# Kernel tuning notes

Hardware: AMD Instinct MI355X
Metric: run time of the kernel (lower is better)

## Reference

```python
import jax, jax.numpy as jnp
import numpy as np

N, E, H, L = 50000, 1_600_000, 128, 3


def _ln(x, g, b, eps=1e-5):
    m = x.mean(-1, keepdims=True)
    v = x.var(-1, keepdims=True)
    return (x - m) / jnp.sqrt(v + eps) * g + b


def _mlp2(inp, w1, b1, g, be, w2, b2):
    # Linear -> LayerNorm -> SiLU -> (Dropout=identity in eval) -> Linear
    h = inp @ w1 + b1
    h = jax.nn.silu(_ln(h, g, be))
    return h @ w2 + b2


def setup_inputs() -> dict:
    key = jax.random.key(0)
    ks = jax.random.split(key, 16)
    s = 0.05
    inp = {
        'x': jax.random.normal(ks[0], (N, 7), jnp.float32),
        'pos': jax.random.normal(ks[1], (N, 3), jnp.float32),
        'edge_index': jax.random.randint(ks[2], (2, E), 0, N, jnp.int64),
        'enc_w1': jax.random.normal(ks[3], (7, H)) * s,
        'enc_b1': jnp.zeros((H,)),
        'enc_g': jnp.ones((H,)),
        'enc_be': jnp.zeros((H,)),
        'enc_w2': jax.random.normal(ks[4], (H, H)) * s,
        'enc_b2': jnp.zeros((H,)),
        'e_w1': jax.random.normal(ks[5], (L, 2 * H + 5, H)) * s,
        'e_b1': jnp.zeros((L, H)),
        'e_g': jnp.ones((L, H)),
        'e_be': jnp.zeros((L, H)),
        'e_w2': jax.random.normal(ks[6], (L, H, H)) * s,
        'e_b2': jnp.zeros((L, H)),
        'n_w1': jax.random.normal(ks[7], (L, 2 * H, H)) * s,
        'n_b1': jnp.zeros((L, H)),
        'n_g': jnp.ones((L, H)),
        'n_be': jnp.zeros((L, H)),
        'n_w2': jax.random.normal(ks[8], (L, H, H)) * s,
        'n_b2': jnp.zeros((L, H)),
        'ln_g': jnp.ones((L, H)),
        'ln_b': jnp.zeros((L, H)),
        'dec_w1': jax.random.normal(ks[9], (H, H)) * s,
        'dec_b1': jnp.zeros((H,)),
        'dec_w2': jax.random.normal(ks[10], (H, H // 2)) * s,
        'dec_b2': jnp.zeros((H // 2,)),
        'dec_w3': jax.random.normal(ks[11], (H // 2, 6)) * s,
        'dec_b3': jnp.zeros((6,)),
    }
    return inp


def reference(x, pos, edge_index, enc_w1, enc_b1, enc_g, enc_be, enc_w2, enc_b2,
              e_w1, e_b1, e_g, e_be, e_w2, e_b2,
              n_w1, n_b1, n_g, n_be, n_w2, n_b2,
              ln_g, ln_b, dec_w1, dec_b1, dec_w2, dec_b2, dec_w3, dec_b3):
    n_nodes = x.shape[0]
    row, col = edge_index[0], edge_index[1]  # row=source(j), col=target(i)

    # physics edge features: [dist, direction(3), 1/r^2]
    diff = pos[col] - pos[row]                          # (E,3)
    dist = jnp.linalg.norm(diff, axis=-1, keepdims=True) + 1e-8
    edge_attr = jnp.concatenate([dist, diff / dist, 1.0 / (dist ** 2 + 1e-6)], -1)

    h = _mlp2(x, enc_w1, enc_b1, enc_g, enc_be, enc_w2, enc_b2)  # (N,H)

    for l in range(L):
        # message: cat(x_i, x_j, edge_attr) -> edge MLP
        msg_in = jnp.concatenate([h[col], h[row], edge_attr], -1)  # (E,2H+5)
        msg = _mlp2(msg_in, e_w1[l], e_b1[l], e_g[l], e_be[l], e_w2[l], e_b2[l])
        # scatter-add aggregate to targets
        aggr = jax.ops.segment_sum(msg, col, num_segments=n_nodes)  # (N,H)
        # update: cat(x, aggr) -> node MLP, then residual + LayerNorm
        h_new = _mlp2(jnp.concatenate([h, aggr], -1),
                      n_w1[l], n_b1[l], n_g[l], n_be[l], n_w2[l], n_b2[l])
        h = _ln(h + h_new, ln_g[l], ln_b[l])

    d = jax.nn.silu(h @ dec_w1 + dec_b1)
    d = jax.nn.silu(d @ dec_w2 + dec_b2)
    delta = d @ dec_w3 + dec_b3                                  # (N,6)
    return x[:, :6] + delta
```

## Files before the change

### kernel.cpp

```cpp
#include <hip/hip_runtime.h>

typedef unsigned short u16;
typedef unsigned int u32;
typedef __bf16 bf16x8 __attribute__((ext_vector_type(8)));
typedef float f32x4 __attribute__((ext_vector_type(4)));
typedef float f32x2 __attribute__((ext_vector_type(2)));

#define AS_STRIDE 136

__device__ __forceinline__ u16 f2bf1(float f) {
  union { __bf16 h; u16 u; } c; c.h = (__bf16)f; return c.u;
}
__device__ __forceinline__ u32 cvt2bf(float a, float b) {
  union { __bf16 h[2]; u32 u; } c; c.h[0] = (__bf16)a; c.h[1] = (__bf16)b; return c.u;
}
__device__ __forceinline__ float bf2f(u16 u) {
  union { u32 u; float f; } v; v.u = ((u32)u) << 16; return v.f;
}
__device__ __forceinline__ float silu_f(float a) {
  return a * __builtin_amdgcn_rcpf(1.f + __expf(-a));
}
__device__ __forceinline__ float rsq_f(float x) {
  return __builtin_amdgcn_rsqf(x);
}
__device__ __forceinline__ f32x2 unpk2(u32 p) {
  union { u32 u; float f; } a, b;
  a.u = p << 16; b.u = p & 0xffff0000u;
  return (f32x2){a.f, b.f};
}
__device__ __forceinline__ int permP(int i) {
  return ((i >> 2) & 3) * 16 + ((i >> 4) & 3) * 4 + (i & 3);
}

__global__ void edge_hist(const int* __restrict__ edst, int E, int* __restrict__ cnt) {
  int i = blockIdx.x * blockDim.x + threadIdx.x;
  if (i < E) atomicAdd(&cnt[edst[i]], 1);
}

__global__ __launch_bounds__(1024)
void scan_kernel(const int* __restrict__ cnt, int* __restrict__ cursor, int Nn) {
  __shared__ int part[1024];
  int t = threadIdx.x;
  int per = (Nn + 1023) / 1024;
  int b = t * per;
  int s = 0;
  for (int i = 0; i < per; i++) { int idx = b + i; if (idx < Nn) s += cnt[idx]; }
  part[t] = s;
  __syncthreads();
  for (int d = 1; d < 1024; d <<= 1) {
    int v = (t >= d) ? part[t - d] : 0;
    __syncthreads();
    part[t] += v;
    __syncthreads();
  }
  int excl = (t == 0) ? 0 : part[t - 1];
  for (int i = 0; i < per; i++) {
    int idx = b + i;
    if (idx < Nn) { cursor[idx] = excl; excl += cnt[idx]; }
  }
}

__global__ void edge_scatter(const int* __restrict__ esrc, const int* __restrict__ edst,
                             int E, int* __restrict__ cursor,
                             int* __restrict__ ssrc, int* __restrict__ sdst) {
  int i = blockIdx.x * blockDim.x + threadIdx.x;
  if (i < E) {
    int d = edst[i];
    int p = atomicAdd(&cursor[d], 1);
    ssrc[p] = esrc[i];
    sdst[p] = d;
  }
}

__global__ void prep_weights(const float* __restrict__ e_w1, const float* __restrict__ e_w2,
                             const float* __restrict__ n_w1, const float* __restrict__ n_w2,
                             u16* __restrict__ eW1T, u16* __restrict__ eW2T,
                             u16* __restrict__ nW1T, u16* __restrict__ nW2T) {
  int i = blockIdx.x * blockDim.x + threadIdx.x;
  const int s1 = 3 * 128 * 256;
  const int s2 = 3 * 128 * 128;
  if (i < s1) {
    int l = i / 32768, r = i % 32768, n = r >> 8, k = r & 255;
    eW1T[i] = f2bf1(e_w1[l * 33408 + k * 128 + n]);
  } else if (i < s1 + s2) {
    int j = i - s1; int l = j / 16384, r = j % 16384, n = r >> 7, k = r & 127;
    eW2T[j] = f2bf1(e_w2[l * 16384 + k * 128 + n]);
  } else if (i < s1 + s2 + s1) {
    int j = i - s1 - s2; int l = j / 32768, r = j % 32768, n = r >> 8, k = r & 255;
    nW1T[j] = f2bf1(n_w1[l * 32768 + k * 128 + n]);
  } else if (i < 2 * s1 + 2 * s2) {
    int j = i - 2 * s1 - s2; int l = j / 16384, r = j % 16384, n = r >> 7, k = r & 127;
    nW2T[j] = f2bf1(n_w2[l * 16384 + k * 128 + n]);
  }
}

__global__ void prep_weights2(const float* __restrict__ enc_w1, const float* __restrict__ enc_w2,
                              const float* __restrict__ dec_w1, const float* __restrict__ dec_w2,
                              const float* __restrict__ dec_w3,
                              u16* __restrict__ encW1T, u16* __restrict__ encW2T,
                              u16* __restrict__ decW1T, u16* __restrict__ decW2T,
                              u16* __restrict__ decW3T) {
  int i = blockIdx.x * blockDim.x + threadIdx.x;
  if (i < 4096) {
    int n = i >> 5, k = i & 31;
    encW1T[i] = (k < 7) ? f2bf1(enc_w1[k * 128 + n]) : (u16)0;
  } else if (i < 20480) {
    int j = i - 4096; int n = j >> 7, k = j & 127;
    encW2T[j] = f2bf1(enc_w2[k * 128 + n]);
  } else if (i < 36864) {
    int j = i - 20480; int n = j >> 7, k = j & 127;
    decW1T[j] = f2bf1(dec_w1[k * 128 + n]);
  } else if (i < 45056) {
    int j = i - 36864; int n = j >> 7, k = j & 127;
    decW2T[j] = f2bf1(dec_w2[k * 64 + n]);
  } else if (i < 46080) {
    int j = i - 45056; int n = j >> 6, k = j & 63;
    decW3T[j] = (n < 6) ? f2bf1(dec_w3[k * 6 + n]) : (u16)0;
  }
}

__global__ __launch_bounds__(256, 4)
void encoder_mfma(const float* __restrict__ x,
                  const u16* __restrict__ W1T,
                  const float* __restrict__ b1,
                  const float* __restrict__ g, const float* __restrict__ be,
                  const u16* __restrict__ W2T,
                  const float* __restrict__ b2,
                  const u16* __restrict__ eW1T0,
                  const float* __restrict__ eb10,
                  u16* __restrict__ hbf, u16* __restrict__ hd_all,
                  u16* __restrict__ hs_all, int Nn) {
  __shared__ __align__(16) u16 As[64 * 40];
  __shared__ __align__(16) u16 ts[64 * AS_STRIDE];
  const int tid = threadIdx.x;
  const int m0 = blockIdx.x * 64;
  const int w = tid >> 6, lane = tid & 63, quad = lane >> 4, l16 = lane & 15;
  const int c0w = w * 32;

  if (tid < 64) {
    int node = m0 + tid; if (node >= Nn) node = Nn - 1;
    union { u16 us[32]; uint4 v[4]; } pk;
    #pragma unroll
    for (int k = 0; k < 32; k++) pk.us[k] = 0;
    #pragma unroll
    for (int k = 0; k < 7; k++) pk.us[k] = f2bf1(x[node * 7 + k]);
    #pragma unroll
    for (int k = 0; k < 4; k++) *(uint4*)(As + tid * 40 + k * 8) = pk.v[k];
  }
  __syncthreads();

  f32x4 acc[4][2];
  #pragma unroll
  for (int rt = 0; rt < 4; rt++)
    #pragma unroll
    for (int ct = 0; ct < 2; ct++)
      acc[rt][ct] = (f32x4){0.f, 0.f, 0.f, 0.f};
  {
    const int kl = quad * 8;
    bf16x8 af[4];
    #pragma unroll
    for (int rt = 0; rt < 4; rt++)
      af[rt] = *(const bf16x8*)(As + (rt * 16 + l16) * 40 + kl);
    #pragma unroll
    for (int ct = 0; ct < 2; ct++) {
      bf16x8 bfv = *(const bf16x8*)(W1T + (c0w + ct * 16 + l16) * 32 + kl);
      #pragma unroll
      for (int rt = 0; rt < 4; rt++)
        acc[rt][ct] = __builtin_amdgcn_mfma_f32_16x16x32_bf16(af[rt], bfv, acc[rt][ct], 0, 0, 0);
    }
  }
  #pragma unroll
  for (int ct = 0; ct < 2; ct++) {
    int n = c0w + ct * 16 + l16;
    float b1v = b1[n];
    #pragma unroll
    for (int rt = 0; rt < 4; rt++)
      #pragma unroll
      for (int r = 0; r < 4; r++)
        ts[(rt * 16 + quad * 4 + r) * AS_STRIDE + n] = f2bf1(acc[rt][ct][r] + b1v);
  }
  __syncthreads();

  {
    int row = tid >> 2, sub = tid & 3;
    float s = 0.f, sq = 0.f, vals[32];
    #pragma unroll
    for (int i = 0; i < 32; i++) {
      float v = bf2f(ts[row * AS_STRIDE + sub + i * 4]);
      vals[i] = v; s += v; sq += v * v;
    }
    s += __shfl_xor(s, 1); sq += __shfl_xor(sq, 1);
    s += __shfl_xor(s, 2); sq += __shfl_xor(sq, 2);
    float mean = s * (1.f / 128.f);
    float rstd = rsq_f(sq * (1.f / 128.f) - mean * mean + 1e-5f);
    #pragma unroll
    for (int i = 0; i < 32; i++) {
      int c = sub + i * 4;
      float a = (vals[i] - mean) * rstd * g[c] + be[c];
      ts[row * AS_STRIDE + c] = f2bf1(silu_f(a));
    }
  }
  __syncthreads();

  f32x4 acc2[4][2];
  #pragma unroll
  for (int rt = 0; rt < 4; rt++)
    #pragma unroll
    for (int ct = 0; ct < 2; ct++)
      acc2[rt][ct] = (f32x4){0.f, 0.f, 0.f, 0.f};
  #pragma unroll
  for (int kk = 0; kk < 4; kk++) {
    const int kl = kk * 32 + quad * 8;
    bf16x8 af[4];
    #pragma unroll
    for (int rt = 0; rt < 4; rt++)
      af[rt] = *(const bf16x8*)(ts + (rt * 16 + l16) * AS_STRIDE + kl);
    #pragma unroll
    for (int ct = 0; ct < 2; ct++) {
      bf16x8 bfv = *(const bf16x8*)(W2T + (size_t)(c0w + ct * 16 + l16) * 128 + kl);
      #pragma unroll
      for (int rt = 0; rt < 4; rt++)
        acc2[rt][ct] = __builtin_amdgcn_mfma_f32_16x16x32_bf16(af[rt], bfv, acc2[rt][ct], 0, 0, 0);
    }
  }
  __syncthreads();
  #pragma unroll
  for (int ct = 0; ct < 2; ct++) {
    int n = c0w + ct * 16 + l16;
    float b2v = b2[n];
    #pragma unroll
    for (int rt = 0; rt < 4; rt++)
      #pragma unroll
      for (int r = 0; r < 4; r++) {
        int m = rt * 16 + quad * 4 + r;
        int node = m0 + m;
        u16 hb = f2bf1(acc2[rt][ct][r] + b2v);
        ts[m * AS_STRIDE + n] = hb;
        if (node < Nn) hbf[(size_t)node * 128 + n] = hb;
      }
  }
  __syncthreads();

  {
    f32x4 ah[4][2];
    #pragma unroll
    for (int rt = 0; rt < 4; rt++)
      #pragma unroll
      for (int ct = 0; ct < 2; ct++)
        ah[rt][ct] = (f32x4){0.f, 0.f, 0.f, 0.f};
    #pragma unroll
    for (int kk = 0; kk < 4; kk++) {
      const int kl = kk * 32 + quad * 8;
      bf16x8 af[4];
      #pragma unroll
      for (int rt = 0; rt < 4; rt++)
        af[rt] = *(const bf16x8*)(ts + (rt * 16 + l16) * AS_STRIDE + kl);
      #pragma unroll
      for (int ct = 0; ct < 2; ct++) {
        bf16x8 bd = *(const bf16x8*)(eW1T0 + (size_t)(c0w + ct * 16 + l16) * 256 + kl);
        #pragma unroll
        for (int rt = 0; rt < 4; rt++)
          ah[rt][ct] = __builtin_amdgcn_mfma_f32_16x16x32_bf16(af[rt], bd, ah[rt][ct], 0, 0, 0);
      }
    }
    #pragma unroll
    for (int ct = 0; ct < 2; ct++) {
      int n = c0w + ct * 16 + l16;
      float b1v = eb10[n];
      #pragma unroll
      for (int rt = 0; rt < 4; rt++)
        #pragma unroll
        for (int r = 0; r < 4; r++) {
          int node = m0 + rt * 16 + quad * 4 + r;
          if (node < Nn) hd_all[(size_t)node * 128 + n] = f2bf1(ah[rt][ct][r] + b1v);
        }
    }
    #pragma unroll
    for (int rt = 0; rt < 4; rt++)
      #pragma unroll
      for (int ct = 0; ct < 2; ct++)
        ah[rt][ct] = (f32x4){0.f, 0.f, 0.f, 0.f};
    #pragma unroll
    for (int kk = 0; kk < 4; kk++) {
      const int kl = kk * 32 + quad * 8;
      bf16x8 af[4];
      #pragma unroll
      for (int rt = 0; rt < 4; rt++)
        af[rt] = *(const bf16x8*)(ts + (rt * 16 + l16) * AS_STRIDE + kl);
      #pragma unroll
      for (int ct = 0; ct < 2; ct++) {
        bf16x8 bs = *(const bf16x8*)(eW1T0 + (size_t)(c0w + ct * 16 + l16) * 256 + 128 + kl);
        #pragma unroll
        for (int rt = 0; rt < 4; rt++)
          ah[rt][ct] = __builtin_amdgcn_mfma_f32_16x16x32_bf16(af[rt], bs, ah[rt][ct], 0, 0, 0);
      }
    }
    #pragma unroll
    for (int ct = 0; ct < 2; ct++) {
      int n = c0w + ct * 16 + l16;
      #pragma unroll
      for (int rt = 0; rt < 4; rt++)
        #pragma unroll
        for (int r = 0; r < 4; r++) {
          int node = m0 + rt * 16 + quad * 4 + r;
          if (node < Nn) hs_all[(size_t)node * 128 + n] = f2bf1(ah[rt][ct][r]);
        }
    }
  }
}

__global__ __launch_bounds__(256, 6)
void edge_mlp_kernel(const int* __restrict__ ssrc, const int* __restrict__ sdst,
                     const float* __restrict__ pos,
                     const u16* __restrict__ hd_all, const u16* __restrict__ hs_all,
                     const float* __restrict__ w1cF,
                     const float* __restrict__ g, const float* __restrict__ be,
                     const u16* __restrict__ W2T,
                     const float* __restrict__ b2,
                     float* __restrict__ aggr) {
  __shared__ int s_dst[64];
  __shared__ __align__(16) float s_ea[64 * 8];
  __shared__ __align__(16) float s_w1c[5 * 128];
  __shared__ __align__(16) u16 s_t[64 * AS_STRIDE];

  const int tid = threadIdx.x;
  const int bid = blockIdx.x;
  const int e0 = ((bid & 7) * (gridDim.x >> 3) + (bid >> 3)) * 64;
  const int w = tid >> 6, lane = tid & 63, quad = lane >> 4, l16 = lane & 15;
  const int c0w = w * 32;
  const int rg = tid >> 4, cg = tid & 15;
  const int c0 = cg * 8;

  int pdst[4], psrc[4];
  #pragma unroll
  for (int rr = 0; rr < 4; rr++) {
    int j = permP(rg * 4 + rr);
    pdst[rr] = sdst[e0 + j];
    psrc[rr] = ssrc[e0 + j];
  }
  uint4 hd4[4], hs4[4];
  #pragma unroll
  for (int rr = 0; rr < 4; rr++) {
    hd4[rr] = *(const uint4*)(hd_all + (size_t)pdst[rr] * 128 + c0);
    hs4[rr] = *(const uint4*)(hs_all + (size_t)psrc[rr] * 128 + c0);
  }
  asm volatile("" ::: "memory");

  if (tid < 64) {
    int jp = permP(tid);
    int src = ssrc[e0 + jp], dst = sdst[e0 + jp];
    s_dst[tid] = sdst[e0 + tid];
    float dx = pos[dst * 3 + 0] - pos[src * 3 + 0];
    float dy = pos[dst * 3 + 1] - pos[src * 3 + 1];
    float dz = pos[dst * 3 + 2] - pos[src * 3 + 2];
    float dist = sqrtf(dx * dx + dy * dy + dz * dz) + 1e-8f;
    float inv = __builtin_amdgcn_rcpf(dist);
    s_ea[tid * 8 + 0] = dist;
    s_ea[tid * 8 + 1] = dx * inv;
    s_ea[tid * 8 + 2] = dy * inv;
    s_ea[tid * 8 + 3] = dz * inv;
    s_ea[tid * 8 + 4] = __builtin_amdgcn_rcpf(dist * dist + 1e-6f);
  }
  if (tid < 160) *(float4*)(s_w1c + tid * 4) = *(const float4*)(w1cF + tid * 4);
  __syncthreads();

  {
    f32x2 t2a[4][4];
    #pragma unroll
    for (int rr = 0; rr < 4; rr++) {
      u32 hp[4] = {hd4[rr].x, hd4[rr].y, hd4[rr].z, hd4[rr].w};
      u32 sp[4] = {hs4[rr].x, hs4[rr].y, hs4[rr].z, hs4[rr].w};
      #pragma unroll
      for (int p = 0; p < 4; p++)
        t2a[rr][p] = unpk2(hp[p]) + unpk2(sp[p]);
    }
    #pragma unroll
    for (int k = 0; k < 5; k++) {
      f32x4 wa = *(const f32x4*)(s_w1c + k * 128 + c0);
      f32x4 wb = *(const f32x4*)(s_w1c + k * 128 + c0 + 4);
      f32x2 wk0 = (f32x2){wa[0], wa[1]}, wk1 = (f32x2){wa[2], wa[3]};
      f32x2 wk2 = (f32x2){wb[0], wb[1]}, wk3 = (f32x2){wb[2], wb[3]};
      #pragma unroll
      for (int rr = 0; rr < 4; rr++) {
        float e = s_ea[(rg * 4 + rr) * 8 + k];
        f32x2 ev = (f32x2){e, e};
        t2a[rr][0] += ev * wk0;
        t2a[rr][1] += ev * wk1;
        t2a[rr][2] += ev * wk2;
        t2a[rr][3] += ev * wk3;
      }
    }
    f32x2 g2[4], be2[4];
    {
      f32x4 ga = *(const f32x4*)(g + c0), gb = *(const f32x4*)(g + c0 + 4);
      f32x4 ba = *(const f32x4*)(be + c0), bb = *(const f32x4*)(be + c0 + 4);
      g2[0] = (f32x2){ga[0], ga[1]}; g2[1] = (f32x2){ga[2], ga[3]};
      g2[2] = (f32x2){gb[0], gb[1]}; g2[3] = (f32x2){gb[2], gb[3]};
      be2[0] = (f32x2){ba[0], ba[1]}; be2[1] = (f32x2){ba[2], ba[3]};
      be2[2] = (f32x2){bb[0], bb[1]}; be2[3] = (f32x2){bb[2], bb[3]};
    }
    #pragma unroll
    for (int rr = 0; rr < 4; rr++) {
      int m = rg * 4 + rr;
      f32x2 sm2 = (f32x2){0.f, 0.f}, sq2 = (f32x2){0.f, 0.f};
      #pragma unroll
      for (int p = 0; p < 4; p++) {
        sm2 += t2a[rr][p];
        sq2 += t2a[rr][p] * t2a[rr][p];
      }
      float sm = sm2[0] + sm2[1], sq = sq2[0] + sq2[1];
      sm += __shfl_xor(sm, 1);  sq += __shfl_xor(sq, 1);
      sm += __shfl_xor(sm, 2);  sq += __shfl_xor(sq, 2);
      sm += __shfl_xor(sm, 4);  sq += __shfl_xor(sq, 4);
      sm += __shfl_xor(sm, 8);  sq += __shfl_xor(sq, 8);
      float mean = sm * (1.f / 128.f);
      float rstd = rsq_f(sq * (1.f / 128.f) - mean * mean + 1e-5f);
      f32x2 sc = (f32x2){rstd, rstd};
      f32x2 ofs = (f32x2){-mean * rstd, -mean * rstd};
      float o[8];
      #pragma unroll
      for (int p = 0; p < 4; p++) {
        f32x2 a = t2a[rr][p] * sc + ofs;
        a = a * g2[p] + be2[p];
        o[2 * p]     = silu_f(a[0]);
        o[2 * p + 1] = silu_f(a[1]);
      }
      uint4 st;
      st.x = cvt2bf(o[0], o[1]); st.y = cvt2bf(o[2], o[3]);
      st.z = cvt2bf(o[4], o[5]); st.w = cvt2bf(o[6], o[7]);
      *(uint4*)(s_t + m * AS_STRIDE + c0) = st;
    }
  }
  __syncthreads();

  f32x4 acc2[4][2];
  #pragma unroll
  for (int rt = 0; rt < 4; rt++)
    #pragma unroll
    for (int ct = 0; ct < 2; ct++)
      acc2[rt][ct] = (f32x4){0.f, 0.f, 0.f, 0.f};

  #pragma unroll
  for (int kk = 0; kk < 4; kk++) {
    const int kl = kk * 32 + quad * 8;
    bf16x8 af[4];
    #pragma unroll
    for (int rt = 0; rt < 4; rt++)
      af[rt] = *(const bf16x8*)(s_t + (rt * 16 + l16) * AS_STRIDE + kl);
    #pragma unroll
    for (int ct = 0; ct < 2; ct++) {
      bf16x8 bfv = *(const bf16x8*)(W2T + (size_t)(c0w + ct * 16 + l16) * 128 + kl);
      #pragma unroll
      for (int rt = 0; rt < 4; rt++)
        acc2[rt][ct] = __builtin_amdgcn_mfma_f32_16x16x32_bf16(af[rt], bfv, acc2[rt][ct], 0, 0, 0);
    }
  }

  {
    int dv[16];
    #pragma unroll
    for (int j = 0; j < 16; j++) dv[j] = s_dst[quad * 16 + j];

    #pragma unroll
    for (int ct = 0; ct < 2; ct++) {
      const int n = c0w + ct * 16 + l16;
      const float b2v = b2[n];
      float* ap = aggr + n;
      int cur = dv[0];
      float run = 0.f;
      #pragma unroll
      for (int j = 0; j < 16; j++) {
        if (dv[j] != cur) {
          atomicAdd(ap + (size_t)cur * 128, run);
          run = 0.f; cur = dv[j];
        }
        run += acc2[j >> 2][ct][j & 3] + b2v;
      }
      atomicAdd(ap + (size_t)cur * 128, run);
    }
  }
}

__global__ __launch_bounds__(256, 4)
void node_mlp_kernel(u16* __restrict__ hbf, float* __restrict__ aggr,
                     const u16* __restrict__ W1T, const float* __restrict__ b1,
                     const float* __restrict__ g, const float* __restrict__ be,
                     const u16* __restrict__ W2T, const float* __restrict__ b2,
                     const float* __restrict__ lng, const float* __restrict__ lnb,
                     const u16* __restrict__ W1Tn, const float* __restrict__ b1n,
                     u16* __restrict__ hd_all, u16* __restrict__ hs_all,
                     const float* __restrict__ x,
                     const u16* __restrict__ dW1T, const float* __restrict__ db1,
                     const u16* __restrict__ dW2T, const float* __restrict__ db2,
                     const u16* __restrict__ dW3T, const float* __restrict__ db3,
                     float* __restrict__ out,
                     int Nn) {
  __shared__ __align__(16) u16 As[128 * AS_STRIDE];
  u16* t_su = As;
  u16* u_su = As + 64 * AS_STRIDE;

  const int tid = threadIdx.x;
  const int m0 = blockIdx.x * 64;
  const int w = tid >> 6, lane = tid & 63, quad = lane >> 4, l16 = lane & 15;
  const int c0w = w * 32;

  {
    int r = tid >> 4, c8 = (tid & 15) * 8;
    const float4 z4 = {0.f, 0.f, 0.f, 0.f};
    #pragma unroll
    for (int rp = 0; rp < 4; rp++) {
      int m = rp * 16 + r;
      int node = m0 + m; if (node >= Nn) node = Nn - 1;
      *(uint4*)(As + m * AS_STRIDE + c8) = *(const uint4*)(hbf + (size_t)node * 128 + c8);
      float* ap = aggr + (size_t)node * 128 + c8;
      float4 f0 = *(const float4*)ap;
      float4 f1 = *(const float4*)(ap + 4);
      uint4 pk;
      pk.x = cvt2bf(f0.x, f0.y); pk.y = cvt2bf(f0.z, f0.w);
      pk.z = cvt2bf(f1.x, f1.y); pk.w = cvt2bf(f1.z, f1.w);
      *(uint4*)(As + (64 + m) * AS_STRIDE + c8) = pk;
      *(float4*)ap = z4;
      *(float4*)(ap + 4) = z4;
    }
  }
  __syncthreads();

  f32x4 acc[4][2];
  #pragma unroll
  for (int rt = 0; rt < 4; rt++)
    #pragma unroll
    for (int ct = 0; ct < 2; ct++)
      acc[rt][ct] = (f32x4){0.f, 0.f, 0.f, 0.f};

  #pragma unroll
  for (int kk = 0; kk < 8; kk++) {
    const u16* Ab = As + (kk < 4 ? 0 : 64 * AS_STRIDE);
    const int kl = (kk & 3) * 32 + quad * 8;
    bf16x8 af[4];
    #pragma unroll
    for (int rt = 0; rt < 4; rt++)
      af[rt] = *(const bf16x8*)(Ab + (rt * 16 + l16) * AS_STRIDE + kl);
    const int kg = kk * 32 + quad * 8;
    #pragma unroll
    for (int ct = 0; ct < 2; ct++) {
      bf16x8 bfv = *(const bf16x8*)(W1T + (size_t)(c0w + ct * 16 + l16) * 256 + kg);
      #pragma unroll
      for (int rt = 0; rt < 4; rt++)
        acc[rt][ct] = __builtin_amdgcn_mfma_f32_16x16x32_bf16(af[rt], bfv, acc[rt][ct], 0, 0, 0);
    }
  }

  float b1v[2];
  #pragma unroll
  for (int ct = 0; ct < 2; ct++) b1v[ct] = b1[c0w + ct * 16 + l16];
  __syncthreads();

  #pragma unroll
  for (int rt = 0; rt < 4; rt++)
    #pragma unroll
    for (int ct = 0; ct < 2; ct++) {
      int n = c0w + ct * 16 + l16;
      #pragma unroll
      for (int r = 0; r < 4; r++)
        t_su[(rt * 16 + quad * 4 + r) * AS_STRIDE + n] = f2bf1(acc[rt][ct][r] + b1v[ct]);
    }
  __syncthreads();

  {
    int row = tid >> 2, sub = tid & 3;
    float s = 0.f, sq = 0.f, vals[32];
    #pragma unroll
    for (int i = 0; i < 32; i++) {
      float v = bf2f(t_su[row * AS_STRIDE + sub + i * 4]);
      vals[i] = v; s += v; sq += v * v;
    }
    s += __shfl_xor(s, 1); sq += __shfl_xor(sq, 1);
    s += __shfl_xor(s, 2); sq += __shfl_xor(sq, 2);
    float mean = s * (1.f / 128.f);
    float rstd = rsq_f(sq * (1.f / 128.f) - mean * mean + 1e-5f);
    #pragma unroll
    for (int i = 0; i < 32; i++) {
      int c = sub + i * 4;
      float a = (vals[i] - mean) * rstd * g[c] + be[c];
      u_su[row * AS_STRIDE + c] = f2bf1(silu_f(a));
    }
  }
  __syncthreads();

  f32x4 acc2[4][2];
  #pragma unroll
  for (int rt = 0; rt < 4; rt++)
    #pragma unroll
    for (int ct = 0; ct < 2; ct++)
      acc2[rt][ct] = (f32x4){0.f, 0.f, 0.f, 0.f};

  #pragma unroll
  for (int kk = 0; kk < 4; kk++) {
    const int kl = kk * 32 + quad * 8;
    bf16x8 af[4];
    #pragma unroll
    for (int rt = 0; rt < 4; rt++)
      af[rt] = *(const bf16x8*)(u_su + (rt * 16 + l16) * AS_STRIDE + kl);
    #pragma unroll
    for (int ct = 0; ct < 2; ct++) {
      bf16x8 bfv = *(const bf16x8*)(W2T + (size_t)(c0w + ct * 16 + l16) * 128 + kl);
      #pragma unroll
      for (int rt = 0; rt < 4; rt++)
        acc2[rt][ct] = __builtin_amdgcn_mfma_f32_16x16x32_bf16(af[rt], bfv, acc2[rt][ct], 0, 0, 0);
    }
  }
  __syncthreads();

  #pragma unroll
  for (int ct = 0; ct < 2; ct++) {
    int n = c0w + ct * 16 + l16;
    float b2v = b2[n];
    #pragma unroll
    for (int rt = 0; rt < 4; rt++)
      #pragma unroll
      for (int r = 0; r < 4; r++) {
        int m = rt * 16 + quad * 4 + r;
        int node = m0 + m; if (node >= Nn) node = Nn - 1;
        t_su[m * AS_STRIDE + n] =
            f2bf1(acc2[rt][ct][r] + b2v + bf2f(hbf[(size_t)node * 128 + n]));
      }
  }
  __syncthreads();

  {
    int row = tid >> 2, sub = tid & 3;
    int node = m0 + row;
    float s = 0.f, sq = 0.f, vals[32];
    #pragma unroll
    for (int i = 0; i < 32; i++) {
      float v = bf2f(t_su[row * AS_STRIDE + sub + i * 4]);
      vals[i] = v; s += v; sq += v * v;
    }
    s += __shfl_xor(s, 1); sq += __shfl_xor(sq, 1);
    s += __shfl_xor(s, 2); sq += __shfl_xor(sq, 2);
    float mean = s * (1.f / 128.f);
    float rstd = rsq_f(sq * (1.f / 128.f) - mean * mean + 1e-5f);
    #pragma unroll
    for (int i = 0; i < 32; i++) {
      int c = sub + i * 4;
      float v = (vals[i] - mean) * rstd * lng[c] + lnb[c];
      u16 hb = f2bf1(v);
      t_su[row * AS_STRIDE + c] = hb;
      if (node < Nn) hbf[(size_t)node * 128 + c] = hb;
    }
  }

  if (W1Tn != nullptr) {
    __syncthreads();
    f32x4 ah[4][2];
    #pragma unroll
    for (int rt = 0; rt < 4; rt++)
      #pragma unroll
      for (int ct = 0; ct < 2; ct++)
        ah[rt][ct] = (f32x4){0.f, 0.f, 0.f, 0.f};
    #pragma unroll
    for (int kk = 0; kk < 4; kk++) {
      const int kl = kk * 32 + quad * 8;
      bf16x8 af[4];
      #pragma unroll
      for (int rt = 0; rt < 4; rt++)
        af[rt] = *(const bf16x8*)(t_su + (rt * 16 + l16) * AS_STRIDE + kl);
      #pragma unroll
      for (int ct = 0; ct < 2; ct++) {
        bf16x8 bd = *(const bf16x8*)(W1Tn + (size_t)(c0w + ct * 16 + l16) * 256 + kl);
        #pragma unroll
        for (int rt = 0; rt < 4; rt++)
          ah[rt][ct] = __builtin_amdgcn_mfma_f32_16x16x32_bf16(af[rt], bd, ah[rt][ct], 0, 0, 0);
      }
    }
    #pragma unroll
    for (int ct = 0; ct < 2; ct++) {
      int n = c0w + ct * 16 + l16;
      float bv = b1n[n];
      #pragma unroll
      for (int rt = 0; rt < 4; rt++)
        #pragma unroll
        for (int r = 0; r < 4; r++) {
          int node = m0 + rt * 16 + quad * 4 + r;
          if (node < Nn) hd_all[(size_t)node * 128 + n] = f2bf1(ah[rt][ct][r] + bv);
        }
    }
    #pragma unroll
    for (int rt = 0; rt < 4; rt++)
      #pragma unroll
      for (int ct = 0; ct < 2; ct++)
        ah[rt][ct] = (f32x4){0.f, 0.f, 0.f, 0.f};
    #pragma unroll
    for (int kk = 0; kk < 4; kk++) {
      const int kl = kk * 32 + quad * 8;
      bf16x8 af[4];
      #pragma unroll
      for (int rt = 0; rt < 4; rt++)
        af[rt] = *(const bf16x8*)(t_su + (rt * 16 + l16) * AS_STRIDE + kl);
      #pragma unroll
      for (int ct = 0; ct < 2; ct++) {
        bf16x8 bs = *(const bf16x8*)(W1Tn + (size_t)(c0w + ct * 16 + l16) * 256 + 128 + kl);
        #pragma unroll
        for (int rt = 0; rt < 4; rt++)
          ah[rt][ct] = __builtin_amdgcn_mfma_f32_16x16x32_bf16(af[rt], bs, ah[rt][ct], 0, 0, 0);
      }
    }
    #pragma unroll
    for (int ct = 0; ct < 2; ct++) {
      int n = c0w + ct * 16 + l16;
      #pragma unroll
      for (int rt = 0; rt < 4; rt++)
        #pragma unroll
        for (int r = 0; r < 4; r++) {
          int node = m0 + rt * 16 + quad * 4 + r;
          if (node < Nn) hs_all[(size_t)node * 128 + n] = f2bf1(ah[rt][ct][r]);
        }
    }
  }

  if (dW1T != nullptr) {
    __syncthreads();
    f32x4 da[4][2];
    #pragma unroll
    for (int rt = 0; rt < 4; rt++)
      #pragma unroll
      for (int ct = 0; ct < 2; ct++)
        da[rt][ct] = (f32x4){0.f, 0.f, 0.f, 0.f};
    #pragma unroll
    for (int kk = 0; kk < 4; kk++) {
      const int kl = kk * 32 + quad * 8;
      bf16x8 af[4];
      #pragma unroll
      for (int rt = 0; rt < 4; rt++)
        af[rt] = *(const bf16x8*)(t_su + (rt * 16 + l16) * AS_STRIDE + kl);
      #pragma unroll
      for (int ct = 0; ct < 2; ct++) {
        bf16x8 bfv = *(const bf16x8*)(dW1T + (size_t)(c0w + ct * 16 + l16) * 128 + kl);
        #pragma unroll
        for (int rt = 0; rt < 4; rt++)
          da[rt][ct] = __builtin_amdgcn_mfma_f32_16x16x32_bf16(af[rt], bfv, da[rt][ct], 0, 0, 0);
      }
    }
    __syncthreads();
    #pragma unroll
    for (int ct = 0; ct < 2; ct++) {
      int n = c0w + ct * 16 + l16;
      float bv = db1[n];
      #pragma unroll
      for (int rt = 0; rt < 4; rt++)
        #pragma unroll
        for (int r = 0; r < 4; r++)
          u_su[(rt * 16 + quad * 4 + r) * AS_STRIDE + n] = f2bf1(silu_f(da[rt][ct][r] + bv));
    }
    __syncthreads();
    {
      const int c0b = w * 16;
      f32x4 a2[4];
      #pragma unroll
      for (int rt = 0; rt < 4; rt++) a2[rt] = (f32x4){0.f, 0.f, 0.f, 0.f};
      #pragma unroll
      for (int kk = 0; kk < 4; kk++) {
        const int kl = kk * 32 + quad * 8;
        bf16x8 af[4];
        #pragma unroll
        for (int rt = 0; rt < 4; rt++)
          af[rt] = *(const bf16x8*)(u_su + (rt * 16 + l16) * AS_STRIDE + kl);
        bf16x8 bfv = *(const bf16x8*)(dW2T + (size_t)(c0b + l16) * 128 + kl);
        #pragma unroll
        for (int rt = 0; rt < 4; rt++)
          a2[rt] = __builtin_amdgcn_mfma_f32_16x16x32_bf16(af[rt], bfv, a2[rt], 0, 0, 0);
      }
      float bv = db2[c0b + l16];
      #pragma unroll
      for (int rt = 0; rt < 4; rt++)
        #pragma unroll
        for (int r = 0; r < 4; r++)
          t_su[(rt * 16 + quad * 4 + r) * 72 + c0b + l16] = f2bf1(silu_f(a2[rt][r] + bv));
    }
    __syncthreads();
    if (w == 0) {
      f32x4 a3[4];
      #pragma unroll
      for (int rt = 0; rt < 4; rt++) a3[rt] = (f32x4){0.f, 0.f, 0.f, 0.f};
      #pragma unroll
      for (int kk = 0; kk < 2; kk++) {
        const int kl = kk * 32 + quad * 8;
        bf16x8 af[4];
        #pragma unroll
        for (int rt = 0; rt < 4; rt++)
          af[rt] = *(const bf16x8*)(t_su + (rt * 16 + l16) * 72 + kl);
        bf16x8 bfv = *(const bf16x8*)(dW3T + l16 * 64 + kl);
        #pragma unroll
        for (int rt = 0; rt < 4; rt++)
          a3[rt] = __builtin_amdgcn_mfma_f32_16x16x32_bf16(af[rt], bfv, a3[rt], 0, 0, 0);
      }
      if (l16 < 6) {
        float bv = db3[l16];
        #pragma unroll
        for (int rt = 0; rt < 4; rt++)
          #pragma unroll
          for (int r = 0; r < 4; r++) {
            int node = m0 + rt * 16 + quad * 4 + r;
            if (node < Nn)
              out[(size_t)node * 6 + l16] = a3[rt][r] + bv + x[node * 7 + l16];
          }
      }
    }
  }
}

extern "C" void kernel_launch(void* const* d_in, const int* in_sizes, int n_in,
                              void* d_out, int out_size, void* d_ws, size_t ws_size,
                              hipStream_t stream) {
  const float* x      = (const float*)d_in[0];
  const float* pos    = (const float*)d_in[1];
  const int*   eidx   = (const int*)d_in[2];
  const float* enc_w1 = (const float*)d_in[3];
  const float* enc_b1 = (const float*)d_in[4];
  const float* enc_g  = (const float*)d_in[5];
  const float* enc_be = (const float*)d_in[6];
  const float* enc_w2 = (const float*)d_in[7];
  const float* enc_b2 = (const float*)d_in[8];
  const float* e_w1   = (const float*)d_in[9];
  const float* e_b1   = (const float*)d_in[10];
  const float* e_g    = (const float*)d_in[11];
  const float* e_be   = (const float*)d_in[12];
  const float* e_w2   = (const float*)d_in[13];
  const float* e_b2   = (const float*)d_in[14];
  const float* n_w1   = (const float*)d_in[15];
  const float* n_b1   = (const float*)d_in[16];
  const float* n_g    = (const float*)d_in[17];
  const float* n_be   = (const float*)d_in[18];
  const float* n_w2   = (const float*)d_in[19];
  const float* n_b2   = (const float*)d_in[20];
  const float* ln_g   = (const float*)d_in[21];
  const float* ln_b   = (const float*)d_in[22];
  const float* dec_w1 = (const float*)d_in[23];
  const float* dec_b1 = (const float*)d_in[24];
  const float* dec_w2 = (const float*)d_in[25];
  const float* dec_b2 = (const float*)d_in[26];
  const float* dec_w3 = (const float*)d_in[27];
  const float* dec_b3 = (const float*)d_in[28];

  const int N = in_sizes[0] / 7;
  const int E = in_sizes[2] / 2;

  char* ws = (char*)d_ws;
  size_t off = 0;
  u16*   hbf    = (u16*)(ws + off);   off += (size_t)N * 128 * 2;
  u16*   hd_all = (u16*)(ws + off);   off += (size_t)N * 128 * 2;
  u16*   hs_all = (u16*)(ws + off);   off += (size_t)N * 128 * 2;
  float* aggr   = (float*)(ws + off); off += (size_t)N * 128 * 4;
  u16* eW1T = (u16*)(ws + off); off += 3 * 128 * 256 * 2;
  u16* eW2T = (u16*)(ws + off); off += 3 * 128 * 128 * 2;
  u16* nW1T = (u16*)(ws + off); off += 3 * 128 * 256 * 2;
  u16* nW2T = (u16*)(ws + off); off += 3 * 128 * 128 * 2;
  u16* encW1T = (u16*)(ws + off); off += 128 * 32 * 2;
  u16* encW2T = (u16*)(ws + off); off += 128 * 128 * 2;
  u16* decW1T = (u16*)(ws + off); off += 128 * 128 * 2;
  u16* decW2T = (u16*)(ws + off); off += 64 * 128 * 2;
  u16* decW3T = (u16*)(ws + off); off += 16 * 64 * 2;
  int* cnt    = (int*)(ws + off); off += (size_t)N * 4;
  int* cursor = (int*)(ws + off); off += (size_t)N * 4;
  int* ssrc   = (int*)(ws + off); off += (size_t)E * 4;
  int* sdst   = (int*)(ws + off); off += (size_t)E * 4;

  hipMemsetAsync(cnt, 0, (size_t)N * 4, stream);
  edge_hist<<<(E + 255) / 256, 256, 0, stream>>>(eidx + E, E, cnt);
  scan_kernel<<<1, 1024, 0, stream>>>(cnt, cursor, N);
  edge_scatter<<<(E + 255) / 256, 256, 0, stream>>>(eidx, eidx + E, E, cursor, ssrc, sdst);

  prep_weights<<<1152, 256, 0, stream>>>(e_w1, e_w2, n_w1, n_w2, eW1T, eW2T, nW1T, nW2T);
  prep_weights2<<<180, 256, 0, stream>>>(enc_w1, enc_w2, dec_w1, dec_w2, dec_w3,
                                         encW1T, encW2T, decW1T, decW2T, decW3T);

  hipMemsetAsync(aggr, 0, (size_t)N * 128 * 4, stream);

  const int nblk = (N + 63) / 64;
  encoder_mfma<<<nblk, 256, 0, stream>>>(x, encW1T, enc_b1, enc_g, enc_be, encW2T, enc_b2,
                                         eW1T, e_b1, hbf, hd_all, hs_all, N);

  for (int l = 0; l < 3; l++) {
    edge_mlp_kernel<<<E / 64, 256, 0, stream>>>(
        ssrc, sdst, pos, hd_all, hs_all,
        e_w1 + (size_t)l * 33408 + 256 * 128,
        e_g + l * 128, e_be + l * 128,
        eW2T + (size_t)l * 128 * 128, e_b2 + l * 128, aggr);
    const u16* W1Tn = (l < 2) ? (eW1T + (size_t)(l + 1) * 128 * 256) : (const u16*)nullptr;
    const bool last = (l == 2);
    node_mlp_kernel<<<nblk, 256, 0, stream>>>(
        hbf, aggr,
        nW1T + (size_t)l * 128 * 256, n_b1 + l * 128, n_g + l * 128, n_be + l * 128,
        nW2T + (size_t)l * 128 * 128, n_b2 + l * 128,
        ln_g + l * 128, ln_b + l * 128,
        W1Tn, e_b1 + ((l + 1) % 3) * 128, hd_all, hs_all,
        x,
        last ? decW1T : (const u16*)nullptr, dec_b1,
        last ? decW2T : (const u16*)nullptr, dec_b2,
        last ? decW3T : (const u16*)nullptr, dec_b3,
        (float*)d_out, N);
  }
}
```

Before: 1.133 ms.

## Make edge MLP wave-local with per-wave LDS slabs and fold bias into node kernel

Restructures the edge kernel so each wave owns 16 edges end to end, using per-wave LDS slabs and an lgkmcnt wait instead of block-wide __syncthreads. The second GEMM now computes all 128 output columns per wave, and its output is staged in LDS as bf16 so lanes can do column-wise segmented atomic reductions. The edge bias b2 is dropped from the per-edge work and added in the node kernel as count[node]*b2. The message is rounded to bf16 before the atomics, which costs precision. All W2 rows are now read per wave, and w1c is read from global memory instead of LDS.

```diff
diff --git a/kernel.cpp b/kernel.cpp
--- a/kernel.cpp
+++ b/kernel.cpp
@@ -27,9 +27,6 @@
   union { u32 u; float f; } a, b;
   a.u = p << 16; b.u = p & 0xffff0000u;
   return (f32x2){a.f, b.f};
-}
-__device__ __forceinline__ int permP(int i) {
-  return ((i >> 2) & 3) * 16 + ((i >> 4) & 3) * 4 + (i & 3);
 }
 
 __global__ void edge_hist(const int* __restrict__ edst, int E, int* __restrict__ cnt) {
@@ -316,53 +313,56 @@
                      const float* __restrict__ w1cF,
                      const float* __restrict__ g, const float* __restrict__ be,
                      const u16* __restrict__ W2T,
-                     const float* __restrict__ b2,
                      float* __restrict__ aggr) {
-  __shared__ int s_dst[64];
-  __shared__ __align__(16) float s_ea[64 * 8];
-  __shared__ __align__(16) float s_w1c[5 * 128];
-  __shared__ __align__(16) u16 s_t[64 * AS_STRIDE];
+  __shared__ int s_dstw[4][16];
+  __shared__ __align__(16) float s_eaw[4][16 * 9];
+  __shared__ __align__(16) u16 s_slab[4][2624];
 
   const int tid = threadIdx.x;
   const int bid = blockIdx.x;
-  const int e0 = ((bid & 7) * (gridDim.x >> 3) + (bid >> 3)) * 64;
+  const int eblk = (bid & 7) * (gridDim.x >> 3) + (bid >> 3);
   const int w = tid >> 6, lane = tid & 63, quad = lane >> 4, l16 = lane & 15;
-  const int c0w = w * 32;
-  const int rg = tid >> 4, cg = tid & 15;
-  const int c0 = cg * 8;
+  const int e0w = eblk * 64 + w * 16;
+  const int c0 = l16 * 8;
+  u16* tile = s_slab[w];
+  u16* msg  = s_slab[w];
+  float* s_ea = s_eaw[w];
 
   int pdst[4], psrc[4];
   #pragma unroll
-  for (int rr = 0; rr < 4; rr++) {
-    int j = permP(rg * 4 + rr);
-    pdst[rr] = sdst[e0 + j];
-    psrc[rr] = ssrc[e0 + j];
+  for (int r = 0; r < 4; r++) {
+    pdst[r] = sdst[e0w + quad * 4 + r];
+    psrc[r] = ssrc[e0w + quad * 4 + r];
   }
   uint4 hd4[4], hs4[4];
   #pragma unroll
-  for (int rr = 0; rr < 4; rr++) {
-    hd4[rr] = *(const uint4*)(hd_all + (size_t)pdst[rr] * 128 + c0);
-    hs4[rr] = *(const uint4*)(hs_all + (size_t)psrc[rr] * 128 + c0);
+  for (int r = 0; r < 4; r++) {
+    hd4[r] = *(const uint4*)(hd_all + (size_t)pdst[r] * 128 + c0);
+    hs4[r] = *(const uint4*)(hs_all + (size_t)psrc[r] * 128 + c0);
   }
   asm volatile("" ::: "memory");
 
-  if (tid < 64) {
-    int jp = permP(tid);
-    int src = ssrc[e0 + jp], dst = sdst[e0 + jp];
-    s_dst[tid] = sdst[e0 + tid];
+  {
+    int je = e0w + l16;
+    int src = ssrc[je], dst = sdst[je];
     float dx = pos[dst * 3 + 0] - pos[src * 3 + 0];
     float dy = pos[dst * 3 + 1] - pos[src * 3 + 1];
     float dz = pos[dst * 3 + 2] - pos[src * 3 + 2];
     float dist = sqrtf(dx * dx + dy * dy + dz * dz) + 1e-8f;
     float inv = __builtin_amdgcn_rcpf(dist);
-    s_ea[tid * 8 + 0] = dist;
-    s_ea[tid * 8 + 1] = dx * inv;
-    s_ea[tid * 8 + 2] = dy * inv;
-    s_ea[tid * 8 + 3] = dz * inv;
-    s_ea[tid * 8 + 4] = __builtin_amdgcn_rcpf(dist * dist + 1e-6f);
-  }
-  if (tid < 160) *(float4*)(s_w1c + tid * 4) = *(const float4*)(w1cF + tid * 4);
-  __syncthreads();
+    if (quad == 0) {
+      s_ea[l16 * 9 + 0] = dist;
+      s_ea[l16 * 9 + 1] = dx * inv;
+      s_ea[l16 * 9 + 2] = dy * inv;
+      s_ea[l16 * 9 + 3] = dz * inv;
+      s_ea[l16 * 9 + 4] = __builtin_amdgcn_rcpf(dist * dist + 1e-6f);
+    }
+    if (l16 == 0) {
+      #pragma unroll
+      for (int r = 0; r < 4; r++) s_dstw[w][quad * 4 + r] = pdst[r];
+    }
+  }
+  asm volatile("s_waitcnt lgkmcnt(0)" ::: "memory");
 
   {
     f32x2 t2a[4][4];
@@ -376,13 +376,13 @@
     }
     #pragma unroll
     for (int k = 0; k < 5; k++) {
-      f32x4 wa = *(const f32x4*)(s_w1c + k * 128 + c0);
-      f32x4 wb = *(const f32x4*)(s_w1c + k * 128 + c0 + 4);
+      f32x4 wa = *(const f32x4*)(w1cF + k * 128 + c0);
+      f32x4 wb = *(const f32x4*)(w1cF + k * 128 + c0 + 4);
       f32x2 wk0 = (f32x2){wa[0], wa[1]}, wk1 = (f32x2){wa[2], wa[3]};
       f32x2 wk2 = (f32x2){wb[0], wb[1]}, wk3 = (f32x2){wb[2], wb[3]};
       #pragma unroll
       for (int rr = 0; rr < 4; rr++) {
-        float e = s_ea[(rg * 4 + rr) * 8 + k];
+        float e = s_ea[(quad * 4 + rr) * 9 + k];
         f32x2 ev = (f32x2){e, e};
         t2a[rr][0] += ev * wk0;
         t2a[rr][1] += ev * wk1;
@@ -401,7 +401,6 @@
     }
     #pragma unroll
     for (int rr = 0; rr < 4; rr++) {
-      int m = rg * 4 + rr;
       f32x2 sm2 = (f32x2){0.f, 0.f}, sq2 = (f32x2){0.f, 0.f};
       #pragma unroll
       for (int p = 0; p < 4; p++) {
@@ -428,61 +427,79 @@
       uint4 st;
       st.x = cvt2bf(o[0], o[1]); st.y = cvt2bf(o[2], o[3]);
       st.z = cvt2bf(o[4], o[5]); st.w = cvt2bf(o[6], o[7]);
-      *(uint4*)(s_t + m * AS_STRIDE + c0) = st;
-    }
-  }
-  __syncthreads();
-
-  f32x4 acc2[4][2];
-  #pragma unroll
-  for (int rt = 0; rt < 4; rt++)
-    #pragma unroll
-    for (int ct = 0; ct < 2; ct++)
-      acc2[rt][ct] = (f32x4){0.f, 0.f, 0.f, 0.f};
-
-  #pragma unroll
-  for (int kk = 0; kk < 4; kk++) {
-    const int kl = kk * 32 + quad * 8;
-    bf16x8 af[4];
-    #pragma unroll
-    for (int rt = 0; rt < 4; rt++)
-      af[rt] = *(const bf16x8*)(s_t + (rt * 16 + l16) * AS_STRIDE + kl);
-    #pragma unroll
-    for (int ct = 0; ct < 2; ct++) {
-      bf16x8 bfv = *(const bf16x8*)(W2T + (size_t)(c0w + ct * 16 + l16) * 128 + kl);
-      #pragma unroll
-      for (int rt = 0; rt < 4; rt++)
-        acc2[rt][ct] = __builtin_amdgcn_mfma_f32_16x16x32_bf16(af[rt], bfv, acc2[rt][ct], 0, 0, 0);
-    }
+      *(uint4*)(tile + (quad * 4 + rr) * AS_STRIDE + c0) = st;
+    }
+  }
+
+  bf16x8 af[4];
+  #pragma unroll
+  for (int kk = 0; kk < 4; kk++)
+    af[kk] = *(const bf16x8*)(tile + l16 * AS_STRIDE + kk * 32 + quad * 8);
+
+  f32x4 acc[8];
+  #pragma unroll
+  for (int ct = 0; ct < 8; ct++) acc[ct] = (f32x4){0.f, 0.f, 0.f, 0.f};
+  #pragma unroll
+  for (int ct = 0; ct < 8; ct++) {
+    #pragma unroll
+    for (int kk = 0; kk < 4; kk++) {
+      bf16x8 bfv = *(const bf16x8*)(W2T + (size_t)(ct * 16 + l16) * 128 + kk * 32 + quad * 8);
+      acc[ct] = __builtin_amdgcn_mfma_f32_16x16x32_bf16(af[kk], bfv, acc[ct], 0, 0, 0);
+    }
+  }
+
+  #pragma unroll
+  for (int ct = 0; ct < 8; ct++) {
+    int n = ct * 16 + l16;
+    uint2 pr;
+    pr.x = cvt2bf(acc[ct][0], acc[ct][1]);
+    pr.y = cvt2bf(acc[ct][2], acc[ct][3]);
+    *(uint2*)(msg + n * 20 + quad * 4) = pr;
   }
 
   {
     int dv[16];
-    #pragma unroll
-    for (int j = 0; j < 16; j++) dv[j] = s_dst[quad * 16 + j];
-
-    #pragma unroll
-    for (int ct = 0; ct < 2; ct++) {
-      const int n = c0w + ct * 16 + l16;
-      const float b2v = b2[n];
-      float* ap = aggr + n;
-      int cur = dv[0];
-      float run = 0.f;
+    {
+      const int4* dp = (const int4*)&s_dstw[w][0];
+      int4 a = dp[0], b = dp[1], c = dp[2], d = dp[3];
+      dv[0] = a.x; dv[1] = a.y; dv[2] = a.z; dv[3] = a.w;
+      dv[4] = b.x; dv[5] = b.y; dv[6] = b.z; dv[7] = b.w;
+      dv[8] = c.x; dv[9] = c.y; dv[10] = c.z; dv[11] = c.w;
+      dv[12] = d.x; dv[13] = d.y; dv[14] = d.z; dv[15] = d.w;
+    }
+    #pragma unroll
+    for (int cc = 0; cc < 2; cc++) {
+      int n = lane + cc * 64;
+      const u16* mp = msg + n * 20;
+      uint2 p0 = *(const uint2*)(mp);
+      uint2 p1 = *(const uint2*)(mp + 4);
+      uint2 p2 = *(const uint2*)(mp + 8);
+      uint2 p3 = *(const uint2*)(mp + 12);
+      float v[16];
+      u32 ws_[8] = {p0.x, p0.y, p1.x, p1.y, p2.x, p2.y, p3.x, p3.y};
+      #pragma unroll
+      for (int q = 0; q < 8; q++) {
+        union { u32 u; float f; } lo, hi;
+        lo.u = ws_[q] << 16; hi.u = ws_[q] & 0xffff0000u;
+        v[2 * q] = lo.f; v[2 * q + 1] = hi.f;
+      }
+      float run = 0.f; int cur = dv[0];
       #pragma unroll
       for (int j = 0; j < 16; j++) {
         if (dv[j] != cur) {
-          atomicAdd(ap + (size_t)cur * 128, run);
+          atomicAdd(aggr + (size_t)cur * 128 + n, run);
           run = 0.f; cur = dv[j];
         }
-        run += acc2[j >> 2][ct][j & 3] + b2v;
-      }
-      atomicAdd(ap + (size_t)cur * 128, run);
+        run += v[j];
+      }
+      atomicAdd(aggr + (size_t)cur * 128 + n, run);
     }
   }
 }
 
 __global__ __launch_bounds__(256, 4)
 void node_mlp_kernel(u16* __restrict__ hbf, float* __restrict__ aggr,
+                     const int* __restrict__ cnt, const float* __restrict__ eb2,
                      const u16* __restrict__ W1T, const float* __restrict__ b1,
                      const float* __restrict__ g, const float* __restrict__ be,
                      const u16* __restrict__ W2T, const float* __restrict__ b2,
@@ -507,14 +524,19 @@
   {
     int r = tid >> 4, c8 = (tid & 15) * 8;
     const float4 z4 = {0.f, 0.f, 0.f, 0.f};
+    const float4 e0 = *(const float4*)(eb2 + c8);
+    const float4 e1 = *(const float4*)(eb2 + c8 + 4);
     #pragma unroll
     for (int rp = 0; rp < 4; rp++) {
       int m = rp * 16 + r;
       int node = m0 + m; if (node >= Nn) node = Nn - 1;
       *(uint4*)(As + m * AS_STRIDE + c8) = *(const uint4*)(hbf + (size_t)node * 128 + c8);
       float* ap = aggr + (size_t)node * 128 + c8;
+      float cf = (float)cnt[node];
       float4 f0 = *(const float4*)ap;
       float4 f1 = *(const float4*)(ap + 4);
+      f0.x += cf * e0.x; f0.y += cf * e0.y; f0.z += cf * e0.z; f0.w += cf * e0.w;
+      f1.x += cf * e1.x; f1.y += cf * e1.y; f1.z += cf * e1.z; f1.w += cf * e1.w;
       uint4 pk;
       pk.x = cvt2bf(f0.x, f0.y); pk.y = cvt2bf(f0.z, f0.w);
       pk.z = cvt2bf(f1.x, f1.y); pk.w = cvt2bf(f1.z, f1.w);
@@ -885,11 +907,11 @@
         ssrc, sdst, pos, hd_all, hs_all,
         e_w1 + (size_t)l * 33408 + 256 * 128,
         e_g + l * 128, e_be + l * 128,
-        eW2T + (size_t)l * 128 * 128, e_b2 + l * 128, aggr);
+        eW2T + (size_t)l * 128 * 128, aggr);
     const u16* W1Tn = (l < 2) ? (eW1T + (size_t)(l + 1) * 128 * 256) : (const u16*)nullptr;
     const bool last = (l == 2);
     node_mlp_kernel<<<nblk, 256, 0, stream>>>(
-        hbf, aggr,
+        hbf, aggr, cnt, e_b2 + l * 128,
         nW1T + (size_t)l * 128 * 256, n_b1 + l * 128, n_g + l * 128, n_be + l * 128,
         nW2T + (size_t)l * 128 * 128, n_b2 + l * 128,
         ln_g + l * 128, ln_b + l * 128,
```

Measured after the change: 1.937 ms. +70.9%, slower.
